# Performance work log

Measured on AMD Instinct MI355X. Metric: run time of the kernel, lower is better.

## Reference

```python
import jax, jax.numpy as jnp
import numpy as np
import math

NUM_HEADS = 16
EMBED_DIM = 1024
DIM_HEAD = EMBED_DIM // NUM_HEADS


def setup_inputs() -> dict:
    key = jax.random.key(0)
    k_x, k_wi, k_bi, k_wo, k_bo = jax.random.split(key, 5)
    B, S, D = 2, 2048, EMBED_DIM
    scale = 1.0 / math.sqrt(D)
    return {
        "x": jax.random.normal(k_x, (B, S, D), dtype=jnp.float32),
        "w_in": jax.random.normal(k_wi, (3 * D, D), dtype=jnp.float32) * scale,
        "b_in": jax.random.normal(k_bi, (3 * D,), dtype=jnp.float32) * 0.02,
        "w_out": jax.random.normal(k_wo, (D, D), dtype=jnp.float32) * scale,
        "b_out": jax.random.normal(k_bo, (D,), dtype=jnp.float32) * 0.02,
    }


def reference(x, w_in, b_in, w_out, b_out):
    B, S, D = x.shape
    H, Dh = NUM_HEADS, DIM_HEAD
    # in_proj: x @ w_in.T + b_in -> chunk into q, k, v
    qkv = jnp.einsum("bsd,ed->bse", x, w_in) + b_in  # [B,S,3D]
    q, k, v = jnp.split(qkv, 3, axis=-1)
    q = q.reshape(B, S, H, Dh).transpose(0, 2, 1, 3)  # [B,H,S,Dh]
    k = k.reshape(B, S, H, Dh).transpose(0, 2, 1, 3)
    v = v.reshape(B, S, H, Dh).transpose(0, 2, 1, 3)
    # scores, causal mask (masked_fill before scaling == after, since -inf/c = -inf)
    scores = jnp.einsum("bhqd,bhkd->bhqk", q, k) / math.sqrt(Dh)
    causal = jnp.triu(jnp.ones((S, S), dtype=bool), k=1)
    scores = jnp.where(causal, -jnp.inf, scores)
    weight = jax.nn.softmax(scores, axis=-1)
    out = jnp.einsum("bhqk,bhkd->bhqd", weight, v)  # [B,H,S,Dh]
    out = out.transpose(0, 2, 1, 3).reshape(B, S, D)
    return jnp.einsum("bsd,ed->bse", out, w_out) + b_out
```

## Files before the change

### kernel.cpp

```cpp
#include <hip/hip_runtime.h>
#include <stdint.h>

typedef unsigned short u16;
typedef float f32x4 __attribute__((ext_vector_type(4)));
typedef __bf16 bf16x8 __attribute__((ext_vector_type(8)));

#define AS1 __attribute__((address_space(1)))
#define AS3 __attribute__((address_space(3)))

#define QK_SCALE 0.18033688011112042f

__device__ __forceinline__ u16 f32_to_bf16(float f) {
    unsigned u = __float_as_uint(f);
    unsigned r = u + 0x7fffu + ((u >> 16) & 1u);
    return (u16)(r >> 16);
}

__device__ __forceinline__ float bf16_f(u16 u) {
    return __uint_as_float(((unsigned)u) << 16);
}

__device__ __forceinline__ void gload_lds16(const u16* g, u16* l) {
    __builtin_amdgcn_global_load_lds((const AS1 unsigned int*)g,
                                     (AS3 unsigned int*)l, 16, 0, 0);
}

__device__ __forceinline__ int swz(int row, int col8) {
    return row * 64 + (((col8 ^ (row & 7)) & 7) << 3);
}
__device__ __forceinline__ int swzv(int row, int col8) {
    return row * 64 + (((col8 ^ row ^ (row >> 3)) & 7) << 3);
}

__global__ __launch_bounds__(256) void cvt_bf16_3(const float4* __restrict__ in0,
                                                  const float4* __restrict__ in1,
                                                  const float4* __restrict__ in2,
                                                  uint2* __restrict__ out,
                                                  int n0, int n1, int ntot) {
    for (int i = blockIdx.x * blockDim.x + threadIdx.x; i < ntot;
         i += gridDim.x * blockDim.x) {
        float4 v;
        if (i < n0) v = in0[i];
        else if (i < n0 + n1) {
            v = in1[i - n0];
            if (((i - n0) >> 8) < 1024) {
                v.x *= QK_SCALE; v.y *= QK_SCALE; v.z *= QK_SCALE; v.w *= QK_SCALE;
            }
        } else v = in2[i - n0 - n1];
        uint2 o;
        o.x = (unsigned)f32_to_bf16(v.x) | ((unsigned)f32_to_bf16(v.y) << 16);
        o.y = (unsigned)f32_to_bf16(v.z) | ((unsigned)f32_to_bf16(v.w) << 16);
        out[i] = o;
    }
}

template <int BNT, bool BF16_OUT>
__global__ __launch_bounds__(512, 2) void gemm_ring(const u16* __restrict__ A,
                                                    const u16* __restrict__ B,
                                                    const float* __restrict__ bias,
                                                    void* __restrict__ Cv,
                                                    int M, int N, int K,
                                                    int qcols, float qscale) {
    extern __shared__ u16 lds[];
    constexpr int NACC = BNT / 64;
    constexpr int NCH = (128 + BNT) >> 7;
    constexpr int ASZ = 128 * 32;
    constexpr int BSZ = BNT * 32;
    const int t = threadIdx.x;
    const int l = t & 63, w = t >> 6;
    const int lr = l & 15, lhi = l >> 4;
    const int wm = w >> 2, wn = w & 3;
    const int orig = blockIdx.y * gridDim.x + blockIdx.x;
    const int sid = (orig & 7) * 32 + (orig >> 3);
    const int bm = sid & 31, bn = sid >> 5;

    const u16* Ag = A + (size_t)bm * 128 * K;
    const u16* Bg = B + (size_t)bn * BNT * K;

    auto STAGE = [&](int kt, int slot) {
        u16* As = lds + slot * ASZ;
        u16* Bs = lds + 4 * ASZ + slot * BSZ;
        {
            int c = t, row = c >> 2, cp = c & 3;
            int gc = (cp ^ ((row >> 1) & 3)) << 3;
            gload_lds16(Ag + (size_t)row * K + kt * 32 + gc, As + c * 8);
        }
        #pragma unroll
        for (int i = 0; i < NCH - 1; ++i) {
            int c = i * 512 + t, row = c >> 2, cp = c & 3;
            int gc = (cp ^ ((row >> 1) & 3)) << 3;
            gload_lds16(Bg + (size_t)row * K + kt * 32 + gc, Bs + c * 8);
        }
    };

    f32x4 acc[4][NACC] = {};
    const int NT = K >> 5;
    STAGE(0, 0);
    STAGE(1, 1);
    STAGE(2, 2);

    const int ckey = (lr >> 1) & 3;

    for (int kt = 0; kt < NT; ++kt) {
        if (kt < NT - 2) {
            if constexpr (NCH == 4) asm volatile("s_waitcnt vmcnt(8)" ::: "memory");
            else                    asm volatile("s_waitcnt vmcnt(4)" ::: "memory");
        } else if (kt == NT - 2) {
            if constexpr (NCH == 4) asm volatile("s_waitcnt vmcnt(4)" ::: "memory");
            else                    asm volatile("s_waitcnt vmcnt(2)" ::: "memory");
        } else {
            asm volatile("s_waitcnt vmcnt(0)" ::: "memory");
        }
        __builtin_amdgcn_s_barrier();
        __builtin_amdgcn_sched_barrier(0);

        if (kt + 3 < NT) STAGE(kt + 3, (kt + 3) & 3);

        const u16* As = lds + (kt & 3) * ASZ;
        const u16* Bs = lds + 4 * ASZ + (kt & 3) * BSZ;
        bf16x8 af[4], bfv[NACC];
        #pragma unroll
        for (int m = 0; m < 4; ++m) {
            int row = wm * 64 + m * 16 + lr;
            af[m] = *(const bf16x8*)(As + row * 32 + ((lhi ^ ckey) << 3));
        }
        #pragma unroll
        for (int n = 0; n < NACC; ++n) {
            int row = wn * (BNT / 4) + n * 16 + lr;
            bfv[n] = *(const bf16x8*)(Bs + row * 32 + ((lhi ^ ckey) << 3));
        }
        __builtin_amdgcn_s_setprio(1);
        #pragma unroll
        for (int m = 0; m < 4; ++m)
            #pragma unroll
            for (int n = 0; n < NACC; ++n)
                acc[m][n] = __builtin_amdgcn_mfma_f32_16x16x32_bf16(
                    af[m], bfv[n], acc[m][n], 0, 0, 0);
        __builtin_amdgcn_s_setprio(0);
    }

    const int row0 = bm * 128 + wm * 64 + lhi * 4;
    const int col0 = bn * BNT + wn * (BNT / 4) + lr;
    #pragma unroll
    for (int n = 0; n < NACC; ++n) {
        int col = col0 + n * 16;
        float bv = bias[col];
        if (col < qcols) bv *= qscale;
        #pragma unroll
        for (int m = 0; m < 4; ++m)
            #pragma unroll
            for (int r = 0; r < 4; ++r) {
                int row = row0 + m * 16 + r;
                float v = acc[m][n][r] + bv;
                if constexpr (BF16_OUT)
                    ((u16*)Cv)[(size_t)row * N + col] = f32_to_bf16(v);
                else
                    ((float*)Cv)[(size_t)row * N + col] = v;
            }
    }
}

__device__ __forceinline__ void write_vt(u16* vt, uint4 a, uint4 b, int g, int cl) {
    unsigned aw[4] = {a.x, a.y, a.z, a.w};
    unsigned bw[4] = {b.x, b.y, b.z, b.w};
    #pragma unroll
    for (int j = 0; j < 8; ++j) {
        int dh = cl * 8 + j;
        unsigned sel = (j & 1) ? 0x07060302u : 0x05040100u;
        unsigned v = __builtin_amdgcn_perm(bw[j >> 1], aw[j >> 1], sel);
        *(unsigned*)(vt + swzv(dh, g >> 2) + (2 * g & 7)) = v;
    }
}

__global__ __launch_bounds__(512, 4) void attn_kernel(const u16* __restrict__ qkv,
                                                      u16* __restrict__ out) {
    __shared__ u16 Ks[2][2][64 * 64];
    __shared__ u16 Vt[2][64 * 64];
    __shared__ u16 Ps[8][16 * 64];
    const int t = threadIdx.x;
    const int w = t >> 6, l = t & 63;
    const int lr = l & 15, lhi = l >> 4;
    const int par = w >> 2, wl = w & 3;
    const int tp = t & 255;
    const int orig = blockIdx.x;
    const int sid = (orig & 7) * 64 + (orig >> 3);
    const int bh = sid >> 4, bi = sid & 15;
    const int h = bh & 15, b = bh >> 4;

    const u16* Kg = qkv + ((size_t)(b * 2048)) * 3072 + 1024 + h * 64;
    const u16* Vg = qkv + ((size_t)(b * 2048)) * 3072 + 2048 + h * 64;
    const int vg = tp >> 3, vcl = tp & 7;
    u16* Pw = Ps[w];
    unsigned* Pst = (unsigned*)Pw;
    float2* mlX = (float2*)&Ks[0][0][0];

    #pragma unroll 1
    for (int pass = 0; pass < 2; ++pass) {
        const int qt = pass ? (31 - bi) : bi;
        __syncthreads();

        const u16* Qrow = qkv + ((size_t)(b * 2048 + qt * 64 + wl * 16 + lr)) * 3072 + h * 64;
        bf16x8 qf0 = *(const bf16x8*)(Qrow + lhi * 8);
        bf16x8 qf1 = *(const bf16x8*)(Qrow + 32 + lhi * 8);

        uint4 va = {0, 0, 0, 0}, vbr = {0, 0, 0, 0};
        if (par <= qt) {
            #pragma unroll
            for (int i = 0; i < 2; ++i) {
                int c = i * 256 + tp, r = c >> 3, cl = c & 7;
                gload_lds16(Kg + ((size_t)(par * 64 + r)) * 3072 + ((cl ^ (r & 7)) << 3),
                            &Ks[par][0][c * 8]);
            }
            va = *(const uint4*)(Vg + ((size_t)(par * 64 + 2 * vg)) * 3072 + vcl * 8);
            vbr = *(const uint4*)(Vg + ((size_t)(par * 64 + 2 * vg + 1)) * 3072 + vcl * 8);
            write_vt(Vt[par], va, vbr, vg, vcl);
        }
        __syncthreads();

        f32x4 acc[4] = {};
        float m_run = -1e30f, l_run = 0.f;
        int cur = 0;
        const int nt = (qt >> 1) + 1;

        for (int it = 0; it < nt; ++it) {
            const int t64 = 2 * it + par;
            const bool active = (t64 <= qt);
            const bool pfv = (t64 + 2 <= qt);
            if (pfv) {
                #pragma unroll
                for (int i = 0; i < 2; ++i) {
                    int c = i * 256 + tp, r = c >> 3, cl = c & 7;
                    gload_lds16(Kg + ((size_t)((t64 + 2) * 64 + r)) * 3072 +
                                    ((cl ^ (r & 7)) << 3),
                                &Ks[par][cur ^ 1][c * 8]);
                }
                va = *(const uint4*)(Vg + ((size_t)((t64 + 2) * 64 + 2 * vg)) * 3072 + vcl * 8);
                vbr = *(const uint4*)(Vg + ((size_t)((t64 + 2) * 64 + 2 * vg + 1)) * 3072 + vcl * 8);
            }

            if (active) {
                f32x4 sv[4] = {};
                __builtin_amdgcn_s_setprio(1);
                #pragma unroll
                for (int kks = 0; kks < 2; ++kks) {
                    #pragma unroll
                    for (int n = 0; n < 4; ++n) {
                        bf16x8 kf = *(const bf16x8*)(&Ks[par][cur][swz(n * 16 + lr, kks * 4 + lhi)]);
                        sv[n] = __builtin_amdgcn_mfma_f32_16x16x32_bf16(
                            kf, kks ? qf1 : qf0, sv[n], 0, 0, 0);
                    }
                }
                __builtin_amdgcn_s_setprio(0);

                if (t64 == qt) {
                    #pragma unroll
                    for (int n = 0; n < 4; ++n)
                        #pragma unroll
                        for (int r = 0; r < 4; ++r)
                            if ((n * 16 + lhi * 4 + r) > (wl * 16 + lr)) sv[n][r] = -1e30f;
                }
                float t0 = fmaxf(fmaxf(sv[0][0], sv[0][1]), fmaxf(sv[0][2], sv[0][3]));
                float t1 = fmaxf(fmaxf(sv[1][0], sv[1][1]), fmaxf(sv[1][2], sv[1][3]));
                float t2 = fmaxf(fmaxf(sv[2][0], sv[2][1]), fmaxf(sv[2][2], sv[2][3]));
                float t3 = fmaxf(fmaxf(sv[3][0], sv[3][1]), fmaxf(sv[3][2], sv[3][3]));
                float mx = fmaxf(fmaxf(t0, t1), fmaxf(t2, t3));
                mx = fmaxf(mx, __shfl_xor(mx, 16, 64));
                mx = fmaxf(mx, __shfl_xor(mx, 32, 64));

                if (__any(mx > m_run + 8.f)) {
                    float mn = fmaxf(m_run, mx);
                    float alpha = exp2f(m_run - mn);
                    m_run = mn;
                    l_run *= alpha;
                    #pragma unroll
                    for (int r = 0; r < 4; ++r) {
                        float ar = __shfl(alpha, lhi * 4 + r, 16);
                        #pragma unroll
                        for (int n = 0; n < 4; ++n) acc[n][r] *= ar;
                    }
                }

                float rs = 0.f;
                #pragma unroll
                for (int n = 0; n < 4; ++n)
                    #pragma unroll
                    for (int r = 0; r < 4; ++r) {
                        float pe = exp2f(sv[n][r] - m_run);
                        sv[n][r] = pe;
                        rs += pe;
                    }
                l_run += rs;

                #pragma unroll
                for (int n = 0; n < 4; ++n) {
                    union { uint2 u2; __bf16 hh[4]; } pk;
                    pk.hh[0] = (__bf16)sv[n][0];
                    pk.hh[1] = (__bf16)sv[n][1];
                    pk.hh[2] = (__bf16)sv[n][2];
                    pk.hh[3] = (__bf16)sv[n][3];
                    int pp = 8 * n + 2 * lhi;
                    *(uint2*)&Pst[lr * 32 + (((pp >> 2) ^ (lr & 7)) << 2) + (pp & 3)] = pk.u2;
                }

                __builtin_amdgcn_s_setprio(1);
                #pragma unroll
                for (int kks = 0; kks < 2; ++kks) {
                    bf16x8 pa = *(const bf16x8*)(Pw + lr * 64 +
                                                 (((kks * 4 + lhi) ^ (lr & 7)) << 3));
                    #pragma unroll
                    for (int n = 0; n < 4; ++n) {
                        bf16x8 vb = *(const bf16x8*)(&Vt[par][swzv(n * 16 + lr, kks * 4 + lhi)]);
                        acc[n] = __builtin_amdgcn_mfma_f32_16x16x32_bf16(pa, vb, acc[n], 0, 0, 0);
                    }
                }
                __builtin_amdgcn_s_setprio(0);
            }

            __syncthreads();
            if (pfv) write_vt(Vt[par], va, vbr, vg, vcl);
            __syncthreads();
            cur ^= 1;
        }

        l_run += __shfl_xor(l_run, 16, 64);
        l_run += __shfl_xor(l_run, 32, 64);

        if (par == 1) {
            if (lhi == 0) mlX[wl * 16 + lr] = make_float2(m_run, l_run);
            #pragma unroll
            for (int r = 0; r < 4; ++r)
                #pragma unroll
                for (int n = 0; n < 4; ++n)
                    Pw[(lhi * 4 + r) * 64 + n * 16 + lr] = f32_to_bf16(acc[n][r]);
        }
        __syncthreads();
        if (par == 0) {
            float2 m1l1 = mlX[wl * 16 + lr];
            float m = fmaxf(m_run, m1l1.x);
            float e0 = exp2f(m_run - m), e1 = exp2f(m1l1.x - m);
            float inv = 1.0f / (l_run * e0 + m1l1.y * e1);
            float c0 = e0 * inv, c1 = e1 * inv;
            const u16* Pq = Ps[4 + wl];
            #pragma unroll
            for (int r = 0; r < 4; ++r) {
                float c0r = __shfl(c0, lhi * 4 + r, 16);
                float c1r = __shfl(c1, lhi * 4 + r, 16);
                int qg = qt * 64 + wl * 16 + lhi * 4 + r;
                size_t base = ((size_t)(b * 2048 + qg)) * 1024 + h * 64;
                #pragma unroll
                for (int n = 0; n < 4; ++n) {
                    float v1 = bf16_f(Pq[(lhi * 4 + r) * 64 + n * 16 + lr]);
                    out[base + n * 16 + lr] = f32_to_bf16(acc[n][r] * c0r + v1 * c1r);
                }
            }
        }
    }
}

extern "C" void kernel_launch(void* const* d_in, const int* in_sizes, int n_in,
                              void* d_out, int out_size, void* d_ws, size_t ws_size,
                              hipStream_t stream) {
    const float* x = (const float*)d_in[0];
    const float* w_in = (const float*)d_in[1];
    const float* b_in = (const float*)d_in[2];
    const float* w_out = (const float*)d_in[3];
    const float* b_out = (const float*)d_in[4];
    float* out = (float*)d_out;

    u16* xb = (u16*)d_ws;
    u16* wib = xb + (size_t)4096 * 1024;
    u16* wob = wib + (size_t)3072 * 1024;
    u16* qkvb = wob + (size_t)1024 * 1024;
    u16* attnb = qkvb + (size_t)4096 * 3072;

    const int n0 = 4096 * 1024 / 4, n1 = 3072 * 1024 / 4, n2 = 1024 * 1024 / 4;
    cvt_bf16_3<<<2048, 256, 0, stream>>>((const float4*)x, (const float4*)w_in,
                                         (const float4*)w_out, (uint2*)xb,
                                         n0, n1, n0 + n1 + n2);

    (void)hipFuncSetAttribute((const void*)gemm_ring<384, true>,
                              hipFuncAttributeMaxDynamicSharedMemorySize, 131072);
    (void)hipFuncSetAttribute((const void*)gemm_ring<128, false>,
                              hipFuncAttributeMaxDynamicSharedMemorySize, 65536);

    gemm_ring<384, true><<<dim3(32, 8), 512, 131072, stream>>>(
        xb, wib, b_in, qkvb, 4096, 3072, 1024, 1024, QK_SCALE);
    attn_kernel<<<512, 512, 0, stream>>>(qkvb, attnb);
    gemm_ring<128, false><<<dim3(32, 8), 512, 65536, stream>>>(
        attnb, wob, b_out, out, 4096, 1024, 1024, 0, 1.0f);
}
```

Before: 105.2 us.

## Restructure attention kernel to 128-row Q tiles with 32x32x16 MFMA and register-resident P

The attention kernel now processes one 128-query tile per block instead of two 64-row passes. It uses 32x32x16 bf16 MFMAs with S computed transposed, so the P operand for the PV product is built in registers via v_permlane32_swap instead of round-tripping through a per-wave LDS buffer. The split-KV combine now stages the output in LDS and writes it with coalesced 16-byte stores, and the block-to-work mapping is rebalanced for the causal mask. This is meant to cut LDS traffic and barriers and improve K/V reuse per tile, at the cost of higher register pressure from 16-wide accumulators.

```diff
diff --git a/kernel.cpp b/kernel.cpp
--- a/kernel.cpp
+++ b/kernel.cpp
@@ -3,6 +3,7 @@
 
 typedef unsigned short u16;
 typedef float f32x4 __attribute__((ext_vector_type(4)));
+typedef float f32x16 __attribute__((ext_vector_type(16)));
 typedef __bf16 bf16x8 __attribute__((ext_vector_type(8)));
 
 #define AS1 __attribute__((address_space(1)))
@@ -14,10 +15,6 @@
     unsigned u = __float_as_uint(f);
     unsigned r = u + 0x7fffu + ((u >> 16) & 1u);
     return (u16)(r >> 16);
-}
-
-__device__ __forceinline__ float bf16_f(u16 u) {
-    return __uint_as_float(((unsigned)u) << 16);
 }
 
 __device__ __forceinline__ void gload_lds16(const u16* g, u16* l) {
@@ -176,184 +173,206 @@
                                                       u16* __restrict__ out) {
     __shared__ u16 Ks[2][2][64 * 64];
     __shared__ u16 Vt[2][64 * 64];
-    __shared__ u16 Ps[8][16 * 64];
     const int t = threadIdx.x;
     const int w = t >> 6, l = t & 63;
-    const int lr = l & 15, lhi = l >> 4;
-    const int par = w >> 2, wl = w & 3;
+    const int l31 = l & 31, hi = l >> 5;
+    const int par = w >> 2, wq = w & 3;
     const int tp = t & 255;
-    const int orig = blockIdx.x;
-    const int sid = (orig & 7) * 64 + (orig >> 3);
-    const int bh = sid >> 4, bi = sid & 15;
+    const int x = blockIdx.x & 7, m = blockIdx.x >> 3;
+    const int s5 = m >> 5, g = m & 31;
+    const int qt = s5 ? (15 - (g & 15)) : (g & 15);
+    const int bh = x * 4 + (g >> 4) + 2 * s5;
     const int h = bh & 15, b = bh >> 4;
 
     const u16* Kg = qkv + ((size_t)(b * 2048)) * 3072 + 1024 + h * 64;
     const u16* Vg = qkv + ((size_t)(b * 2048)) * 3072 + 2048 + h * 64;
     const int vg = tp >> 3, vcl = tp & 7;
-    u16* Pw = Ps[w];
-    unsigned* Pst = (unsigned*)Pw;
     float2* mlX = (float2*)&Ks[0][0][0];
-
-    #pragma unroll 1
-    for (int pass = 0; pass < 2; ++pass) {
-        const int qt = pass ? (31 - bi) : bi;
-        __syncthreads();
-
-        const u16* Qrow = qkv + ((size_t)(b * 2048 + qt * 64 + wl * 16 + lr)) * 3072 + h * 64;
-        bf16x8 qf0 = *(const bf16x8*)(Qrow + lhi * 8);
-        bf16x8 qf1 = *(const bf16x8*)(Qrow + 32 + lhi * 8);
-
-        uint4 va = {0, 0, 0, 0}, vbr = {0, 0, 0, 0};
-        if (par <= qt) {
+    u16* Oq = &Ks[1][0][0];
+
+    const int qmine = qt * 128 + wq * 32 + l31;
+    const u16* Qrow = qkv + ((size_t)(b * 2048 + qmine)) * 3072 + h * 64;
+    bf16x8 qv[4];
+    #pragma unroll
+    for (int c = 0; c < 4; ++c)
+        qv[c] = *(const bf16x8*)(Qrow + 16 * c + 8 * hi);
+
+    #pragma unroll
+    for (int i = 0; i < 2; ++i) {
+        int c = i * 256 + tp, r = c >> 3, cl = c & 7;
+        gload_lds16(Kg + ((size_t)(par * 64 + r)) * 3072 + ((cl ^ (r & 7)) << 3),
+                    &Ks[par][0][c * 8]);
+    }
+    {
+        uint4 va0 = *(const uint4*)(Vg + ((size_t)(par * 64 + 2 * vg)) * 3072 + vcl * 8);
+        uint4 vb0 = *(const uint4*)(Vg + ((size_t)(par * 64 + 2 * vg + 1)) * 3072 + vcl * 8);
+        write_vt(Vt[par], va0, vb0, vg, vcl);
+    }
+    __syncthreads();
+
+    f32x16 acc0 = {}, acc1 = {};
+    float m_run = -1e30f, l_run = 0.f;
+    int cur = 0;
+    const int nt = qt + 1;
+
+    for (int it = 0; it < nt; ++it) {
+        const int t64 = 2 * it + par;
+        const bool active = (t64 * 64 <= qt * 128 + wq * 32 + 31);
+        const bool pf = (t64 + 2 <= 2 * qt + 1);
+        uint4 va, vb;
+        if (pf) {
             #pragma unroll
             for (int i = 0; i < 2; ++i) {
                 int c = i * 256 + tp, r = c >> 3, cl = c & 7;
-                gload_lds16(Kg + ((size_t)(par * 64 + r)) * 3072 + ((cl ^ (r & 7)) << 3),
-                            &Ks[par][0][c * 8]);
-            }
-            va = *(const uint4*)(Vg + ((size_t)(par * 64 + 2 * vg)) * 3072 + vcl * 8);
-            vbr = *(const uint4*)(Vg + ((size_t)(par * 64 + 2 * vg + 1)) * 3072 + vcl * 8);
-            write_vt(Vt[par], va, vbr, vg, vcl);
-        }
+                gload_lds16(Kg + ((size_t)((t64 + 2) * 64 + r)) * 3072 +
+                                ((cl ^ (r & 7)) << 3),
+                            &Ks[par][cur ^ 1][c * 8]);
+            }
+            va = *(const uint4*)(Vg + ((size_t)((t64 + 2) * 64 + 2 * vg)) * 3072 + vcl * 8);
+            vb = *(const uint4*)(Vg + ((size_t)((t64 + 2) * 64 + 2 * vg + 1)) * 3072 + vcl * 8);
+        }
+
+        if (active) {
+            const u16* Kc = &Ks[par][cur][0];
+            f32x16 s0, s1;
+            __builtin_amdgcn_s_setprio(1);
+            {
+                f32x16 z16 = {};
+                bf16x8 k0 = *(const bf16x8*)(Kc + swz(l31, hi));
+                bf16x8 k1 = *(const bf16x8*)(Kc + swz(32 + l31, hi));
+                s0 = __builtin_amdgcn_mfma_f32_32x32x16_bf16(k0, qv[0], z16, 0, 0, 0);
+                s1 = __builtin_amdgcn_mfma_f32_32x32x16_bf16(k1, qv[0], z16, 0, 0, 0);
+            }
+            #pragma unroll
+            for (int c = 1; c < 4; ++c) {
+                bf16x8 k0 = *(const bf16x8*)(Kc + swz(l31, 2 * c + hi));
+                bf16x8 k1 = *(const bf16x8*)(Kc + swz(32 + l31, 2 * c + hi));
+                s0 = __builtin_amdgcn_mfma_f32_32x32x16_bf16(k0, qv[c], s0, 0, 0, 0);
+                s1 = __builtin_amdgcn_mfma_f32_32x32x16_bf16(k1, qv[c], s1, 0, 0, 0);
+            }
+            __builtin_amdgcn_s_setprio(0);
+
+            if (t64 >= 2 * qt) {
+                #pragma unroll
+                for (int r = 0; r < 16; ++r) {
+                    int kv = t64 * 64 + (r & 3) + 8 * (r >> 2) + 4 * hi;
+                    if (kv > qmine) s0[r] = -1e30f;
+                    if (kv + 32 > qmine) s1[r] = -1e30f;
+                }
+            }
+            float tm[16];
+            #pragma unroll
+            for (int r = 0; r < 16; ++r) tm[r] = fmaxf(s0[r], s1[r]);
+            #pragma unroll
+            for (int off = 8; off >= 1; off >>= 1)
+                #pragma unroll
+                for (int i2 = 0; i2 < 8; ++i2)
+                    if (i2 < off) tm[i2] = fmaxf(tm[i2], tm[i2 + off]);
+            float mx = fmaxf(tm[0], __shfl_xor(tm[0], 32, 64));
+
+            if (__any(mx > m_run + 8.f)) {
+                float mn = fmaxf(m_run, mx);
+                float alpha = exp2f(m_run - mn);
+                m_run = mn;
+                l_run *= alpha;
+                #pragma unroll
+                for (int r = 0; r < 16; ++r) { acc0[r] *= alpha; acc1[r] *= alpha; }
+            }
+
+            float rs = 0.f;
+            #pragma unroll
+            for (int r = 0; r < 16; ++r) {
+                float a0 = exp2f(s0[r] - m_run);
+                float a1 = exp2f(s1[r] - m_run);
+                s0[r] = a0; s1[r] = a1;
+                rs += a0 + a1;
+            }
+            l_run += rs;
+
+            const u16* Vc = &Vt[par][0];
+            __builtin_amdgcn_s_setprio(1);
+#define PV_STEP(SV, CC)                                                          \
+            {                                                                    \
+                constexpr int base = 8 * ((CC) & 1);                             \
+                union { unsigned u; __bf16 hh[2]; } p0a, p0b, p1a, p1b;          \
+                p0a.hh[0] = (__bf16)SV[base + 0]; p0a.hh[1] = (__bf16)SV[base + 1]; \
+                p0b.hh[0] = (__bf16)SV[base + 2]; p0b.hh[1] = (__bf16)SV[base + 3]; \
+                p1a.hh[0] = (__bf16)SV[base + 4]; p1a.hh[1] = (__bf16)SV[base + 5]; \
+                p1b.hh[0] = (__bf16)SV[base + 6]; p1b.hh[1] = (__bf16)SV[base + 7]; \
+                unsigned w0 = p0a.u, w2 = p1a.u, w1 = p0b.u, w3 = p1b.u;         \
+                asm volatile("v_permlane32_swap_b32 %0, %1" : "+v"(w0), "+v"(w2)); \
+                asm volatile("v_permlane32_swap_b32 %0, %1" : "+v"(w1), "+v"(w3)); \
+                union { uint4 u4; bf16x8 f; } pa;                                \
+                pa.u4 = make_uint4(w0, w1, w2, w3);                              \
+                bf16x8 av0 = *(const bf16x8*)(Vc + swzv(l31, 2 * (CC) + hi));    \
+                bf16x8 av1 = *(const bf16x8*)(Vc + swzv(32 + l31, 2 * (CC) + hi)); \
+                acc0 = __builtin_amdgcn_mfma_f32_32x32x16_bf16(av0, pa.f, acc0, 0, 0, 0); \
+                acc1 = __builtin_amdgcn_mfma_f32_32x32x16_bf16(av1, pa.f, acc1, 0, 0, 0); \
+            }
+            PV_STEP(s0, 0)
+            PV_STEP(s0, 1)
+            PV_STEP(s1, 2)
+            PV_STEP(s1, 3)
+#undef PV_STEP
+            __builtin_amdgcn_s_setprio(0);
+        }
+
         __syncthreads();
-
-        f32x4 acc[4] = {};
-        float m_run = -1e30f, l_run = 0.f;
-        int cur = 0;
-        const int nt = (qt >> 1) + 1;
-
-        for (int it = 0; it < nt; ++it) {
-            const int t64 = 2 * it + par;
-            const bool active = (t64 <= qt);
-            const bool pfv = (t64 + 2 <= qt);
-            if (pfv) {
-                #pragma unroll
-                for (int i = 0; i < 2; ++i) {
-                    int c = i * 256 + tp, r = c >> 3, cl = c & 7;
-                    gload_lds16(Kg + ((size_t)((t64 + 2) * 64 + r)) * 3072 +
-                                    ((cl ^ (r & 7)) << 3),
-                                &Ks[par][cur ^ 1][c * 8]);
-                }
-                va = *(const uint4*)(Vg + ((size_t)((t64 + 2) * 64 + 2 * vg)) * 3072 + vcl * 8);
-                vbr = *(const uint4*)(Vg + ((size_t)((t64 + 2) * 64 + 2 * vg + 1)) * 3072 + vcl * 8);
-            }
-
-            if (active) {
-                f32x4 sv[4] = {};
-                __builtin_amdgcn_s_setprio(1);
-                #pragma unroll
-                for (int kks = 0; kks < 2; ++kks) {
-                    #pragma unroll
-                    for (int n = 0; n < 4; ++n) {
-                        bf16x8 kf = *(const bf16x8*)(&Ks[par][cur][swz(n * 16 + lr, kks * 4 + lhi)]);
-                        sv[n] = __builtin_amdgcn_mfma_f32_16x16x32_bf16(
-                            kf, kks ? qf1 : qf0, sv[n], 0, 0, 0);
-                    }
-                }
-                __builtin_amdgcn_s_setprio(0);
-
-                if (t64 == qt) {
-                    #pragma unroll
-                    for (int n = 0; n < 4; ++n)
-                        #pragma unroll
-                        for (int r = 0; r < 4; ++r)
-                            if ((n * 16 + lhi * 4 + r) > (wl * 16 + lr)) sv[n][r] = -1e30f;
-                }
-                float t0 = fmaxf(fmaxf(sv[0][0], sv[0][1]), fmaxf(sv[0][2], sv[0][3]));
-                float t1 = fmaxf(fmaxf(sv[1][0], sv[1][1]), fmaxf(sv[1][2], sv[1][3]));
-                float t2 = fmaxf(fmaxf(sv[2][0], sv[2][1]), fmaxf(sv[2][2], sv[2][3]));
-                float t3 = fmaxf(fmaxf(sv[3][0], sv[3][1]), fmaxf(sv[3][2], sv[3][3]));
-                float mx = fmaxf(fmaxf(t0, t1), fmaxf(t2, t3));
-                mx = fmaxf(mx, __shfl_xor(mx, 16, 64));
-                mx = fmaxf(mx, __shfl_xor(mx, 32, 64));
-
-                if (__any(mx > m_run + 8.f)) {
-                    float mn = fmaxf(m_run, mx);
-                    float alpha = exp2f(m_run - mn);
-                    m_run = mn;
-                    l_run *= alpha;
-                    #pragma unroll
-                    for (int r = 0; r < 4; ++r) {
-                        float ar = __shfl(alpha, lhi * 4 + r, 16);
-                        #pragma unroll
-                        for (int n = 0; n < 4; ++n) acc[n][r] *= ar;
-                    }
-                }
-
-                float rs = 0.f;
-                #pragma unroll
-                for (int n = 0; n < 4; ++n)
-                    #pragma unroll
-                    for (int r = 0; r < 4; ++r) {
-                        float pe = exp2f(sv[n][r] - m_run);
-                        sv[n][r] = pe;
-                        rs += pe;
-                    }
-                l_run += rs;
-
-                #pragma unroll
-                for (int n = 0; n < 4; ++n) {
-                    union { uint2 u2; __bf16 hh[4]; } pk;
-                    pk.hh[0] = (__bf16)sv[n][0];
-                    pk.hh[1] = (__bf16)sv[n][1];
-                    pk.hh[2] = (__bf16)sv[n][2];
-                    pk.hh[3] = (__bf16)sv[n][3];
-                    int pp = 8 * n + 2 * lhi;
-                    *(uint2*)&Pst[lr * 32 + (((pp >> 2) ^ (lr & 7)) << 2) + (pp & 3)] = pk.u2;
-                }
-
-                __builtin_amdgcn_s_setprio(1);
-                #pragma unroll
-                for (int kks = 0; kks < 2; ++kks) {
-                    bf16x8 pa = *(const bf16x8*)(Pw + lr * 64 +
-                                                 (((kks * 4 + lhi) ^ (lr & 7)) << 3));
-                    #pragma unroll
-                    for (int n = 0; n < 4; ++n) {
-                        bf16x8 vb = *(const bf16x8*)(&Vt[par][swzv(n * 16 + lr, kks * 4 + lhi)]);
-                        acc[n] = __builtin_amdgcn_mfma_f32_16x16x32_bf16(pa, vb, acc[n], 0, 0, 0);
-                    }
-                }
-                __builtin_amdgcn_s_setprio(0);
-            }
-
-            __syncthreads();
-            if (pfv) write_vt(Vt[par], va, vbr, vg, vcl);
-            __syncthreads();
-            cur ^= 1;
-        }
-
-        l_run += __shfl_xor(l_run, 16, 64);
-        l_run += __shfl_xor(l_run, 32, 64);
-
-        if (par == 1) {
-            if (lhi == 0) mlX[wl * 16 + lr] = make_float2(m_run, l_run);
-            #pragma unroll
-            for (int r = 0; r < 4; ++r)
-                #pragma unroll
-                for (int n = 0; n < 4; ++n)
-                    Pw[(lhi * 4 + r) * 64 + n * 16 + lr] = f32_to_bf16(acc[n][r]);
-        }
+        if (pf) write_vt(Vt[par], va, vb, vg, vcl);
         __syncthreads();
-        if (par == 0) {
-            float2 m1l1 = mlX[wl * 16 + lr];
-            float m = fmaxf(m_run, m1l1.x);
-            float e0 = exp2f(m_run - m), e1 = exp2f(m1l1.x - m);
-            float inv = 1.0f / (l_run * e0 + m1l1.y * e1);
-            float c0 = e0 * inv, c1 = e1 * inv;
-            const u16* Pq = Ps[4 + wl];
-            #pragma unroll
-            for (int r = 0; r < 4; ++r) {
-                float c0r = __shfl(c0, lhi * 4 + r, 16);
-                float c1r = __shfl(c1, lhi * 4 + r, 16);
-                int qg = qt * 64 + wl * 16 + lhi * 4 + r;
-                size_t base = ((size_t)(b * 2048 + qg)) * 1024 + h * 64;
-                #pragma unroll
-                for (int n = 0; n < 4; ++n) {
-                    float v1 = bf16_f(Pq[(lhi * 4 + r) * 64 + n * 16 + lr]);
-                    out[base + n * 16 + lr] = f32_to_bf16(acc[n][r] * c0r + v1 * c1r);
-                }
-            }
-        }
+        cur ^= 1;
+    }
+
+    l_run += __shfl_xor(l_run, 32, 64);
+
+    const int qloc = wq * 32 + l31;
+    if (par == 1) {
+        if (hi == 0) mlX[qloc] = make_float2(m_run, l_run);
+#define PUB(ACC, TT)                                                             \
+        _Pragma("unroll")                                                        \
+        for (int a = 0; a < 4; ++a) {                                            \
+            union { uint2 u2; u16 s4[4]; } o;                                    \
+            o.s4[0] = f32_to_bf16(ACC[4 * a + 0]);                               \
+            o.s4[1] = f32_to_bf16(ACC[4 * a + 1]);                               \
+            o.s4[2] = f32_to_bf16(ACC[4 * a + 2]);                               \
+            o.s4[3] = f32_to_bf16(ACC[4 * a + 3]);                               \
+            *(uint2*)&Oq[qloc * 64 + (((4 * (TT) + a) ^ (qloc & 7)) << 3) + 4 * hi] = o.u2; \
+        }
+        PUB(acc0, 0)
+        PUB(acc1, 1)
+#undef PUB
+    }
+    __syncthreads();
+    if (par == 0) {
+        float2 m1 = mlX[qloc];
+        float mm = fmaxf(m_run, m1.x);
+        float e0 = exp2f(m_run - mm), e1 = exp2f(m1.x - mm);
+        float inv = 1.0f / (l_run * e0 + m1.y * e1);
+        float c0 = e0 * inv, c1 = e1 * inv;
+#define CMB(ACC, TT)                                                             \
+        _Pragma("unroll")                                                        \
+        for (int a = 0; a < 4; ++a) {                                            \
+            int ad = qloc * 64 + (((4 * (TT) + a) ^ (qloc & 7)) << 3) + 4 * hi;  \
+            uint2 v1 = *(uint2*)&Oq[ad];                                         \
+            __bf16* h4 = (__bf16*)&v1;                                           \
+            union { uint2 u2; u16 s4[4]; } o;                                    \
+            o.s4[0] = f32_to_bf16(ACC[4 * a + 0] * c0 + (float)h4[0] * c1);      \
+            o.s4[1] = f32_to_bf16(ACC[4 * a + 1] * c0 + (float)h4[1] * c1);      \
+            o.s4[2] = f32_to_bf16(ACC[4 * a + 2] * c0 + (float)h4[2] * c1);      \
+            o.s4[3] = f32_to_bf16(ACC[4 * a + 3] * c0 + (float)h4[3] * c1);      \
+            *(uint2*)&Oq[ad] = o.u2;                                             \
+        }
+        CMB(acc0, 0)
+        CMB(acc1, 1)
+#undef CMB
+    }
+    __syncthreads();
+    #pragma unroll
+    for (int i = 0; i < 2; ++i) {
+        int cch = i * 512 + t;
+        int row = cch >> 3, ch = cch & 7;
+        uint4 v = *(const uint4*)&Oq[row * 64 + ((ch ^ (row & 7)) << 3)];
+        *(uint4*)&out[((size_t)(b * 2048 + qt * 128 + row)) * 1024 + h * 64 + ch * 8] = v;
     }
 }
 
```

Measured after the change: 132.3 us. 1.26x slower.
